# Optimization experiments

Hardware: AMD Instinct MI355X
Metric: run time of the kernel (lower is better)

The kernel has to match this reference:

```python
import jax, jax.numpy as jnp
import numpy as np

N, K, C, HID, G = 100000, 16, 64, 16, 128  # points, knn, channels, mlp hidden, voxel grid


def setup_inputs() -> dict:
    key = jax.random.key(0)
    ks = jax.random.split(key, 8)
    x_F = jax.random.normal(ks[0], (N, C), dtype=jnp.float32)
    idx = jax.random.randint(ks[1], (N, K), 0, N)  # knn neighbor indices

    # --- synthetic unique voxel coords + 3x3x3 sparse-conv neighbor map ---
    rng = np.random.default_rng(0)
    lin = rng.choice(G ** 3, size=N, replace=False)
    lut = np.full(G ** 3, -1, dtype=np.int64)
    lut[lin] = np.arange(N)
    xc, yc, zc = lin // (G * G), (lin // G) % G, lin % G
    nbrs = []
    for dx in (-1, 0, 1):
        for dy in (-1, 0, 1):
            for dz in (-1, 0, 1):
                nx, ny, nz = xc + dx, yc + dy, zc + dz
                valid = (nx >= 0) & (nx < G) & (ny >= 0) & (ny < G) & (nz >= 0) & (nz < G)
                nlin = np.clip(nx, 0, G - 1) * G * G + np.clip(ny, 0, G - 1) * G + np.clip(nz, 0, G - 1)
                nbrs.append(np.where(valid, lut[nlin], -1))
    conv_idx = jnp.asarray(np.stack(nbrs, axis=1))  # (N, 27), -1 = no neighbor voxel

    # --- learned params: shared channel MLP + sparse conv3d(2->1, k=3) weight ---
    W1 = jax.random.normal(ks[2], (C, HID), dtype=jnp.float32) / np.sqrt(C)
    b1 = jnp.zeros((HID,), dtype=jnp.float32)
    W2 = jax.random.normal(ks[3], (HID, C), dtype=jnp.float32) / np.sqrt(HID)
    b2 = jnp.zeros((C,), dtype=jnp.float32)
    conv_w = jax.random.normal(ks[4], (27, 2, 1), dtype=jnp.float32) / np.sqrt(27 * 2)
    return {"x_F": x_F, "W1": W1, "b1": b1, "W2": W2, "b2": b2,
            "conv_w": conv_w, "idx": idx, "conv_idx": conv_idx}


def reference(x_F, W1, b1, W2, b2, conv_w, idx, conv_idx):
    n = x_F.shape[0]

    def mlp(v):
        return jax.nn.relu(v @ W1 + b1) @ W2 + b2

    # channel attention: knn gather -> mean/max pool over k -> shared MLP gate
    g = x_F[idx]                                           # (n, k, c)
    gate = jax.nn.sigmoid(mlp(g.mean(axis=1)) + mlp(g.max(axis=1)))
    outse = x_F * gate                                     # (n, c)

    # spatial attention: pool over flattened (k*c), sparse conv3d(2->1)
    g2 = outse[idx].reshape(n, -1)                         # (n, k*c)
    z = jnp.stack([g2.mean(axis=1), g2.max(axis=1)], axis=1)  # (n, 2)
    mask = (conv_idx >= 0).astype(z.dtype)[..., None]      # (n, 27, 1)
    zn = z[jnp.clip(conv_idx, 0)] * mask                   # (n, 27, 2)
    convf = jnp.einsum('nkc,kco->no', zn, conv_w)          # (n, 1)
    return outse * jax.nn.sigmoid(convf)
```

## Files before the change

### kernel.cpp

```cpp
#include <hip/hip_runtime.h>
#include <math.h>

#define KNN 16
#define CH 64
#define HID 16
#define NEG_BIG (-3.402823466e+38f)

__device__ __forceinline__ float sigmoidf_(float x) {
    return 1.0f / (1.0f + __expf(-x));
}

__device__ __forceinline__ unsigned int pack_bf2(float a, float b) {
    unsigned int ua = __float_as_uint(a), ub = __float_as_uint(b);
    ua = (ua + 0x7FFFu + ((ua >> 16) & 1u)) >> 16;
    ub = (ub + 0x7FFFu + ((ub >> 16) & 1u)) & 0xFFFF0000u;
    return ua | ub;
}

__device__ __forceinline__ float4 bf4_to_f4(unsigned int lo, unsigned int hi) {
    float4 r;
    r.x = __uint_as_float(lo << 16);
    r.y = __uint_as_float(lo & 0xFFFF0000u);
    r.z = __uint_as_float(hi << 16);
    r.w = __uint_as_float(hi & 0xFFFF0000u);
    return r;
}

__device__ __forceinline__ void fold8_2(float A[8], float B[8], int sub) {
    #pragma unroll
    for (int m = 4; m >= 1; m >>= 1) {
        bool hi = (sub & m) != 0;
        #pragma unroll
        for (int i = 0; i < m; ++i) {
            float sA = hi ? A[i] : A[i + m], kA_ = hi ? A[i + m] : A[i];
            A[i] = kA_ + __shfl_xor(sA, m);
            float sB = hi ? B[i] : B[i + m], kB_ = hi ? B[i + m] : B[i];
            B[i] = kB_ + __shfl_xor(sB, m);
        }
    }
}

__global__ __launch_bounds__(256) void kX(const float4* __restrict__ xv,
                                          uint2* __restrict__ xb, int n16) {
    int i = blockIdx.x * 256 + threadIdx.x;
    if (i >= n16) return;
    float4 v = xv[i];
    uint2 r;
    r.x = pack_bf2(v.x, v.y);
    r.y = pack_bf2(v.z, v.w);
    xb[i] = r;
}

__global__ __launch_bounds__(256, 3) void kA(const float4* __restrict__ xv,
        const uint4* __restrict__ xb4,
        const float* __restrict__ W1, const float* __restrict__ b1,
        const float* __restrict__ W2, const float* __restrict__ b2,
        const int2* __restrict__ idx2,
        float4* __restrict__ outse, float2* __restrict__ rowstat, int n) {
    __shared__ float4 w1a[128];
    __shared__ float4 w1b[128];
    __shared__ float4 w2q[256];
    int t = threadIdx.x;
    if (t < 128) {
        int h = t >> 3, s = t & 7;
        float4 a, b;
        a.x = W1[(8 * s + 0) * HID + h];
        a.y = W1[(8 * s + 1) * HID + h];
        a.z = W1[(8 * s + 2) * HID + h];
        a.w = W1[(8 * s + 3) * HID + h];
        b.x = W1[(8 * s + 4) * HID + h];
        b.y = W1[(8 * s + 5) * HID + h];
        b.z = W1[(8 * s + 6) * HID + h];
        b.w = W1[(8 * s + 7) * HID + h];
        w1a[t] = a;
        w1b[t] = b;
    }
    w2q[t] = ((const float4*)W2)[t];
    __syncthreads();

    int p = blockIdx.x * 32 + (t >> 3);
    int sub = t & 7;
    if (p >= n) return;

    int2 jp = idx2[(size_t)p * 8 + sub];
    int jA[8], jB[8];
    #pragma unroll
    for (int s = 0; s < 8; ++s) {
        jA[s] = __shfl(jp.x, s, 8);
        jB[s] = __shfl(jp.y, s, 8);
    }

    uint4 va[8], vb[8];
    #pragma unroll
    for (int s = 0; s < 8; ++s) va[s] = xb4[(size_t)jA[s] * 8 + sub];
    #pragma unroll
    for (int s = 0; s < 8; ++s) vb[s] = xb4[(size_t)jB[s] * 8 + sub];
    float4 own0 = xv[(size_t)p * 16 + 2 * sub];
    float4 own1 = xv[(size_t)p * 16 + 2 * sub + 1];
    float b1a = b1[sub], b1b = b1[sub + 8];
    float4 bq0 = ((const float4*)b2)[2 * sub];
    float4 bq1 = ((const float4*)b2)[2 * sub + 1];
    __builtin_amdgcn_sched_barrier(0);

    float4 sumLo, sumHi, mxLo, mxHi;
    {
        float4 lo = bf4_to_f4(va[0].x, va[0].y);
        float4 hi = bf4_to_f4(va[0].z, va[0].w);
        sumLo = lo; mxLo = lo; sumHi = hi; mxHi = hi;
    }
    #pragma unroll
    for (int s = 1; s < 8; ++s) {
        float4 lo = bf4_to_f4(va[s].x, va[s].y);
        float4 hi = bf4_to_f4(va[s].z, va[s].w);
        sumLo.x += lo.x; sumLo.y += lo.y; sumLo.z += lo.z; sumLo.w += lo.w;
        sumHi.x += hi.x; sumHi.y += hi.y; sumHi.z += hi.z; sumHi.w += hi.w;
        mxLo.x = fmaxf(mxLo.x, lo.x); mxLo.y = fmaxf(mxLo.y, lo.y);
        mxLo.z = fmaxf(mxLo.z, lo.z); mxLo.w = fmaxf(mxLo.w, lo.w);
        mxHi.x = fmaxf(mxHi.x, hi.x); mxHi.y = fmaxf(mxHi.y, hi.y);
        mxHi.z = fmaxf(mxHi.z, hi.z); mxHi.w = fmaxf(mxHi.w, hi.w);
    }
    #pragma unroll
    for (int s = 0; s < 8; ++s) {
        float4 lo = bf4_to_f4(vb[s].x, vb[s].y);
        float4 hi = bf4_to_f4(vb[s].z, vb[s].w);
        sumLo.x += lo.x; sumLo.y += lo.y; sumLo.z += lo.z; sumLo.w += lo.w;
        sumHi.x += hi.x; sumHi.y += hi.y; sumHi.z += hi.z; sumHi.w += hi.w;
        mxLo.x = fmaxf(mxLo.x, lo.x); mxLo.y = fmaxf(mxLo.y, lo.y);
        mxLo.z = fmaxf(mxLo.z, lo.z); mxLo.w = fmaxf(mxLo.w, lo.w);
        mxHi.x = fmaxf(mxHi.x, hi.x); mxHi.y = fmaxf(mxHi.y, hi.y);
        mxHi.z = fmaxf(mxHi.z, hi.z); mxHi.w = fmaxf(mxHi.w, hi.w);
    }
    const float inv_k = 1.0f / KNN;
    float4 meLo = {sumLo.x * inv_k, sumLo.y * inv_k, sumLo.z * inv_k, sumLo.w * inv_k};
    float4 meHi = {sumHi.x * inv_k, sumHi.y * inv_k, sumHi.z * inv_k, sumHi.w * inv_k};

    float Hm_a, Hm_b, Hx_a, Hx_b;
    {
        float A[8], B[8];
        #pragma unroll
        for (int h = 0; h < 8; ++h) {
            float4 wa = w1a[h * 8 + sub], wb = w1b[h * 8 + sub];
            A[h] = meLo.x * wa.x + meLo.y * wa.y + meLo.z * wa.z + meLo.w * wa.w
                 + meHi.x * wb.x + meHi.y * wb.y + meHi.z * wb.z + meHi.w * wb.w;
            float4 wa2 = w1a[(h + 8) * 8 + sub], wb2 = w1b[(h + 8) * 8 + sub];
            B[h] = meLo.x * wa2.x + meLo.y * wa2.y + meLo.z * wa2.z + meLo.w * wa2.w
                 + meHi.x * wb2.x + meHi.y * wb2.y + meHi.z * wb2.z + meHi.w * wb2.w;
        }
        fold8_2(A, B, sub);
        Hm_a = A[0]; Hm_b = B[0];
    }
    {
        float A[8], B[8];
        #pragma unroll
        for (int h = 0; h < 8; ++h) {
            float4 wa = w1a[h * 8 + sub], wb = w1b[h * 8 + sub];
            A[h] = mxLo.x * wa.x + mxLo.y * wa.y + mxLo.z * wa.z + mxLo.w * wa.w
                 + mxHi.x * wb.x + mxHi.y * wb.y + mxHi.z * wb.z + mxHi.w * wb.w;
            float4 wa2 = w1a[(h + 8) * 8 + sub], wb2 = w1b[(h + 8) * 8 + sub];
            B[h] = mxLo.x * wa2.x + mxLo.y * wa2.y + mxLo.z * wa2.z + mxLo.w * wa2.w
                 + mxHi.x * wb2.x + mxHi.y * wb2.y + mxHi.z * wb2.z + mxHi.w * wb2.w;
        }
        fold8_2(A, B, sub);
        Hx_a = A[0]; Hx_b = B[0];
    }
    float H_a = fmaxf(Hm_a + b1a, 0.0f) + fmaxf(Hx_a + b1a, 0.0f);
    float H_b = fmaxf(Hm_b + b1b, 0.0f) + fmaxf(Hx_b + b1b, 0.0f);

    float4 a0 = {0.f, 0.f, 0.f, 0.f}, a1 = {0.f, 0.f, 0.f, 0.f};
    #pragma unroll
    for (int h = 0; h < 8; ++h) {
        float Hh = __shfl(H_a, h, 8);
        float4 w0 = w2q[h * 16 + 2 * sub], w1v = w2q[h * 16 + 2 * sub + 1];
        a0.x += Hh * w0.x; a0.y += Hh * w0.y; a0.z += Hh * w0.z; a0.w += Hh * w0.w;
        a1.x += Hh * w1v.x; a1.y += Hh * w1v.y; a1.z += Hh * w1v.z; a1.w += Hh * w1v.w;
    }
    #pragma unroll
    for (int h = 0; h < 8; ++h) {
        float Hh = __shfl(H_b, h, 8);
        float4 w0 = w2q[(h + 8) * 16 + 2 * sub], w1v = w2q[(h + 8) * 16 + 2 * sub + 1];
        a0.x += Hh * w0.x; a0.y += Hh * w0.y; a0.z += Hh * w0.z; a0.w += Hh * w0.w;
        a1.x += Hh * w1v.x; a1.y += Hh * w1v.y; a1.z += Hh * w1v.z; a1.w += Hh * w1v.w;
    }
    float4 o0, o1;
    o0.x = own0.x * sigmoidf_(a0.x + 2.0f * bq0.x);
    o0.y = own0.y * sigmoidf_(a0.y + 2.0f * bq0.y);
    o0.z = own0.z * sigmoidf_(a0.z + 2.0f * bq0.z);
    o0.w = own0.w * sigmoidf_(a0.w + 2.0f * bq0.w);
    o1.x = own1.x * sigmoidf_(a1.x + 2.0f * bq1.x);
    o1.y = own1.y * sigmoidf_(a1.y + 2.0f * bq1.y);
    o1.z = own1.z * sigmoidf_(a1.z + 2.0f * bq1.z);
    o1.w = own1.w * sigmoidf_(a1.w + 2.0f * bq1.w);
    outse[(size_t)p * 16 + 2 * sub] = o0;
    outse[(size_t)p * 16 + 2 * sub + 1] = o1;

    float sm = (o0.x + o0.y + o0.z + o0.w) + (o1.x + o1.y + o1.z + o1.w);
    float sx = fmaxf(fmaxf(fmaxf(o0.x, o0.y), fmaxf(o0.z, o0.w)),
                     fmaxf(fmaxf(o1.x, o1.y), fmaxf(o1.z, o1.w)));
    #pragma unroll
    for (int m = 4; m >= 1; m >>= 1) {
        sm += __shfl_xor(sm, m);
        sx = fmaxf(sx, __shfl_xor(sx, m));
    }
    if (sub == 0) rowstat[p] = make_float2(sm * (1.0f / 64.0f), sx);
}

__global__ __launch_bounds__(256) void kB(const int4* __restrict__ idxv,
        const float2* __restrict__ rowstat, float2* __restrict__ z, int n) {
    int t = blockIdx.x * 256 + threadIdx.x;
    int i = t >> 1, half = t & 1;
    if (i >= n) return;
    int4 a = idxv[(size_t)i * 4 + half * 2];
    int4 b = idxv[(size_t)i * 4 + half * 2 + 1];
    float2 s0 = rowstat[a.x], s1 = rowstat[a.y], s2 = rowstat[a.z], s3 = rowstat[a.w];
    float2 s4 = rowstat[b.x], s5 = rowstat[b.y], s6 = rowstat[b.z], s7 = rowstat[b.w];
    float zm = (s0.x + s1.x) + (s2.x + s3.x) + ((s4.x + s5.x) + (s6.x + s7.x));
    float zx = fmaxf(fmaxf(fmaxf(s0.y, s1.y), fmaxf(s2.y, s3.y)),
                     fmaxf(fmaxf(s4.y, s5.y), fmaxf(s6.y, s7.y)));
    zm += __shfl_xor(zm, 1);
    zx = fmaxf(zx, __shfl_xor(zx, 1));
    if (half == 0) z[i] = make_float2(zm * (1.0f / 16.0f), zx);
}

__global__ __launch_bounds__(256) void kC(const int* __restrict__ conv_idx,
        const float* __restrict__ conv_w, const float2* __restrict__ z,
        const float4* __restrict__ outse, float4* __restrict__ out, int n) {
    __shared__ float cw[54];
    __shared__ float sgate[256];
    if (threadIdx.x < 54) cw[threadIdx.x] = conv_w[threadIdx.x];
    __syncthreads();
    int base = blockIdx.x * 256;
    int i = base + threadIdx.x;
    if (i < n) {
        float acc = 0.0f;
        #pragma unroll
        for (int k = 0; k < 27; ++k) {
            int j = conv_idx[(size_t)i * 27 + k];
            int jc = j >= 0 ? j : 0;
            float msk = j >= 0 ? 1.0f : 0.0f;
            float2 zz = z[jc];
            acc += msk * (zz.x * cw[2 * k] + zz.y * cw[2 * k + 1]);
        }
        sgate[threadIdx.x] = sigmoidf_(acc);
    }
    __syncthreads();
    int npts = n - base; if (npts > 256) npts = 256;
    int tot = npts * 16;
    for (int q = threadIdx.x; q < tot; q += 256) {
        float s = sgate[q >> 4];
        float4 v = outse[(size_t)base * 16 + q];
        out[(size_t)base * 16 + q] = make_float4(v.x * s, v.y * s, v.z * s, v.w * s);
    }
}

extern "C" void kernel_launch(void* const* d_in, const int* in_sizes, int n_in,
                              void* d_out, int out_size, void* d_ws, size_t ws_size,
                              hipStream_t stream) {
    const float* x_F    = (const float*)d_in[0];
    const float* W1     = (const float*)d_in[1];
    const float* b1     = (const float*)d_in[2];
    const float* W2     = (const float*)d_in[3];
    const float* b2     = (const float*)d_in[4];
    const float* conv_w = (const float*)d_in[5];
    const int*   idx    = (const int*)d_in[6];
    const int*   cidx   = (const int*)d_in[7];
    int n = in_sizes[0] / CH;

    char* ws = (char*)d_ws;
    size_t off = 0;
    uint2*  xb      = (uint2*)(ws + off);  off += (size_t)n * CH * 2;
    float*  outse   = (float*)(ws + off);  off += (size_t)n * CH * 4;
    float2* rowstat = (float2*)(ws + off); off += (size_t)n * 8;
    float2* zz      = (float2*)(ws + off); off += (size_t)n * 8;

    int n16 = n * 16;
    kX<<<(n16 + 255) / 256, 256, 0, stream>>>((const float4*)x_F, xb, n16);
    int blkA = (n + 31) / 32;
    kA<<<blkA, 256, 0, stream>>>((const float4*)x_F, (const uint4*)xb,
                                 W1, b1, W2, b2, (const int2*)idx,
                                 (float4*)outse, rowstat, n);
    int blkB = (2 * n + 255) / 256;
    kB<<<blkB, 256, 0, stream>>>((const int4*)idx, rowstat, zz, n);
    int blkP = (n + 255) / 256;
    kC<<<blkP, 256, 0, stream>>>(cidx, conv_w, zz, (const float4*)outse,
                                 (float4*)d_out, n);
}
```

Before: 171.4 us.

## Fuse four kernels into one persistent cooperative kernel with grid syncs

Replaces the four separate launches (bf16 pack, channel attention, knn row-stat pooling, sparse conv gate) with a single cooperative persistent kernel. The kernel uses grid-stride loops and grid.sync() between phases. The aim is to remove per-launch overhead and inter-kernel gaps. In exchange it adds grid-wide barrier costs and raises the launch-bounds occupancy hint from 3 to 4, which may increase register pressure. The grid size is hardcoded as perCU*256 CUs, which assumes a 256-CU device.

```diff
diff --git a/kernel.cpp b/kernel.cpp
--- a/kernel.cpp
+++ b/kernel.cpp
@@ -1,5 +1,8 @@
 #include <hip/hip_runtime.h>
+#include <hip/hip_cooperative_groups.h>
 #include <math.h>
+
+namespace cg = cooperative_groups;
 
 #define KNN 16
 #define CH 64
@@ -40,27 +43,26 @@
     }
 }
 
-__global__ __launch_bounds__(256) void kX(const float4* __restrict__ xv,
-                                          uint2* __restrict__ xb, int n16) {
-    int i = blockIdx.x * 256 + threadIdx.x;
-    if (i >= n16) return;
-    float4 v = xv[i];
-    uint2 r;
-    r.x = pack_bf2(v.x, v.y);
-    r.y = pack_bf2(v.z, v.w);
-    xb[i] = r;
-}
-
-__global__ __launch_bounds__(256, 3) void kA(const float4* __restrict__ xv,
-        const uint4* __restrict__ xb4,
+__global__ __launch_bounds__(256, 4) void kFused(
+        const float4* __restrict__ xv, uint2* __restrict__ xb,
         const float* __restrict__ W1, const float* __restrict__ b1,
         const float* __restrict__ W2, const float* __restrict__ b2,
-        const int2* __restrict__ idx2,
-        float4* __restrict__ outse, float2* __restrict__ rowstat, int n) {
+        const int* __restrict__ idx, const int* __restrict__ cidx,
+        const float* __restrict__ conv_w,
+        float4* __restrict__ outse, float2* __restrict__ rowstat,
+        float2* __restrict__ zz, float4* __restrict__ out, int n) {
+    cg::grid_group grid = cg::this_grid();
+
     __shared__ float4 w1a[128];
     __shared__ float4 w1b[128];
     __shared__ float4 w2q[256];
+    __shared__ float cw[54];
+    __shared__ float sgate[256];
+
     int t = threadIdx.x;
+    const int gsz = gridDim.x * 256;
+    const int gid = blockIdx.x * 256 + t;
+
     if (t < 128) {
         int h = t >> 3, s = t & 7;
         float4 a, b;
@@ -75,180 +77,198 @@
         w1a[t] = a;
         w1b[t] = b;
     }
+    if (t < 54) cw[t] = conv_w[t];
     w2q[t] = ((const float4*)W2)[t];
     __syncthreads();
 
-    int p = blockIdx.x * 32 + (t >> 3);
-    int sub = t & 7;
-    if (p >= n) return;
-
-    int2 jp = idx2[(size_t)p * 8 + sub];
-    int jA[8], jB[8];
-    #pragma unroll
-    for (int s = 0; s < 8; ++s) {
-        jA[s] = __shfl(jp.x, s, 8);
-        jB[s] = __shfl(jp.y, s, 8);
-    }
-
-    uint4 va[8], vb[8];
-    #pragma unroll
-    for (int s = 0; s < 8; ++s) va[s] = xb4[(size_t)jA[s] * 8 + sub];
-    #pragma unroll
-    for (int s = 0; s < 8; ++s) vb[s] = xb4[(size_t)jB[s] * 8 + sub];
-    float4 own0 = xv[(size_t)p * 16 + 2 * sub];
-    float4 own1 = xv[(size_t)p * 16 + 2 * sub + 1];
-    float b1a = b1[sub], b1b = b1[sub + 8];
-    float4 bq0 = ((const float4*)b2)[2 * sub];
-    float4 bq1 = ((const float4*)b2)[2 * sub + 1];
-    __builtin_amdgcn_sched_barrier(0);
-
-    float4 sumLo, sumHi, mxLo, mxHi;
+    int n16 = n * 16;
+    for (int i = gid; i < n16; i += gsz) {
+        float4 v = xv[i];
+        uint2 r;
+        r.x = pack_bf2(v.x, v.y);
+        r.y = pack_bf2(v.z, v.w);
+        xb[i] = r;
+    }
+    grid.sync();
+
     {
-        float4 lo = bf4_to_f4(va[0].x, va[0].y);
-        float4 hi = bf4_to_f4(va[0].z, va[0].w);
-        sumLo = lo; mxLo = lo; sumHi = hi; mxHi = hi;
-    }
-    #pragma unroll
-    for (int s = 1; s < 8; ++s) {
-        float4 lo = bf4_to_f4(va[s].x, va[s].y);
-        float4 hi = bf4_to_f4(va[s].z, va[s].w);
-        sumLo.x += lo.x; sumLo.y += lo.y; sumLo.z += lo.z; sumLo.w += lo.w;
-        sumHi.x += hi.x; sumHi.y += hi.y; sumHi.z += hi.z; sumHi.w += hi.w;
-        mxLo.x = fmaxf(mxLo.x, lo.x); mxLo.y = fmaxf(mxLo.y, lo.y);
-        mxLo.z = fmaxf(mxLo.z, lo.z); mxLo.w = fmaxf(mxLo.w, lo.w);
-        mxHi.x = fmaxf(mxHi.x, hi.x); mxHi.y = fmaxf(mxHi.y, hi.y);
-        mxHi.z = fmaxf(mxHi.z, hi.z); mxHi.w = fmaxf(mxHi.w, hi.w);
-    }
-    #pragma unroll
-    for (int s = 0; s < 8; ++s) {
-        float4 lo = bf4_to_f4(vb[s].x, vb[s].y);
-        float4 hi = bf4_to_f4(vb[s].z, vb[s].w);
-        sumLo.x += lo.x; sumLo.y += lo.y; sumLo.z += lo.z; sumLo.w += lo.w;
-        sumHi.x += hi.x; sumHi.y += hi.y; sumHi.z += hi.z; sumHi.w += hi.w;
-        mxLo.x = fmaxf(mxLo.x, lo.x); mxLo.y = fmaxf(mxLo.y, lo.y);
-        mxLo.z = fmaxf(mxLo.z, lo.z); mxLo.w = fmaxf(mxLo.w, lo.w);
-        mxHi.x = fmaxf(mxHi.x, hi.x); mxHi.y = fmaxf(mxHi.y, hi.y);
-        mxHi.z = fmaxf(mxHi.z, hi.z); mxHi.w = fmaxf(mxHi.w, hi.w);
-    }
-    const float inv_k = 1.0f / KNN;
-    float4 meLo = {sumLo.x * inv_k, sumLo.y * inv_k, sumLo.z * inv_k, sumLo.w * inv_k};
-    float4 meHi = {sumHi.x * inv_k, sumHi.y * inv_k, sumHi.z * inv_k, sumHi.w * inv_k};
-
-    float Hm_a, Hm_b, Hx_a, Hx_b;
+        const uint4* xb4 = (const uint4*)xb;
+        const int2* idx2 = (const int2*)idx;
+        int sub = t & 7;
+        int nPG = (n + 31) / 32;
+        for (int pg = blockIdx.x; pg < nPG; pg += gridDim.x) {
+            int p = pg * 32 + (t >> 3);
+            if (p < n) {
+                int2 jp = idx2[(size_t)p * 8 + sub];
+                int jA[8], jB[8];
+                #pragma unroll
+                for (int s = 0; s < 8; ++s) {
+                    jA[s] = __shfl(jp.x, s, 8);
+                    jB[s] = __shfl(jp.y, s, 8);
+                }
+                uint4 va[8], vb[8];
+                #pragma unroll
+                for (int s = 0; s < 8; ++s) va[s] = xb4[(size_t)jA[s] * 8 + sub];
+                #pragma unroll
+                for (int s = 0; s < 8; ++s) vb[s] = xb4[(size_t)jB[s] * 8 + sub];
+                float4 own0 = xv[(size_t)p * 16 + 2 * sub];
+                float4 own1 = xv[(size_t)p * 16 + 2 * sub + 1];
+                float b1a = b1[sub], b1b = b1[sub + 8];
+                float4 bq0 = ((const float4*)b2)[2 * sub];
+                float4 bq1 = ((const float4*)b2)[2 * sub + 1];
+                __builtin_amdgcn_sched_barrier(0);
+
+                float4 sumLo, sumHi, mxLo, mxHi;
+                {
+                    float4 lo = bf4_to_f4(va[0].x, va[0].y);
+                    float4 hi = bf4_to_f4(va[0].z, va[0].w);
+                    sumLo = lo; mxLo = lo; sumHi = hi; mxHi = hi;
+                }
+                #pragma unroll
+                for (int s = 1; s < 8; ++s) {
+                    float4 lo = bf4_to_f4(va[s].x, va[s].y);
+                    float4 hi = bf4_to_f4(va[s].z, va[s].w);
+                    sumLo.x += lo.x; sumLo.y += lo.y; sumLo.z += lo.z; sumLo.w += lo.w;
+                    sumHi.x += hi.x; sumHi.y += hi.y; sumHi.z += hi.z; sumHi.w += hi.w;
+                    mxLo.x = fmaxf(mxLo.x, lo.x); mxLo.y = fmaxf(mxLo.y, lo.y);
+                    mxLo.z = fmaxf(mxLo.z, lo.z); mxLo.w = fmaxf(mxLo.w, lo.w);
+                    mxHi.x = fmaxf(mxHi.x, hi.x); mxHi.y = fmaxf(mxHi.y, hi.y);
+                    mxHi.z = fmaxf(mxHi.z, hi.z); mxHi.w = fmaxf(mxHi.w, hi.w);
+                }
+                #pragma unroll
+                for (int s = 0; s < 8; ++s) {
+                    float4 lo = bf4_to_f4(vb[s].x, vb[s].y);
+                    float4 hi = bf4_to_f4(vb[s].z, vb[s].w);
+                    sumLo.x += lo.x; sumLo.y += lo.y; sumLo.z += lo.z; sumLo.w += lo.w;
+                    sumHi.x += hi.x; sumHi.y += hi.y; sumHi.z += hi.z; sumHi.w += hi.w;
+                    mxLo.x = fmaxf(mxLo.x, lo.x); mxLo.y = fmaxf(mxLo.y, lo.y);
+                    mxLo.z = fmaxf(mxLo.z, lo.z); mxLo.w = fmaxf(mxLo.w, lo.w);
+                    mxHi.x = fmaxf(mxHi.x, hi.x); mxHi.y = fmaxf(mxHi.y, hi.y);
+                    mxHi.z = fmaxf(mxHi.z, hi.z); mxHi.w = fmaxf(mxHi.w, hi.w);
+                }
+                const float inv_k = 1.0f / KNN;
+                float4 meLo = {sumLo.x * inv_k, sumLo.y * inv_k, sumLo.z * inv_k, sumLo.w * inv_k};
+                float4 meHi = {sumHi.x * inv_k, sumHi.y * inv_k, sumHi.z * inv_k, sumHi.w * inv_k};
+
+                float Hm_a, Hm_b, Hx_a, Hx_b;
+                {
+                    float A[8], B[8];
+                    #pragma unroll
+                    for (int h = 0; h < 8; ++h) {
+                        float4 wa = w1a[h * 8 + sub], wb = w1b[h * 8 + sub];
+                        A[h] = meLo.x * wa.x + meLo.y * wa.y + meLo.z * wa.z + meLo.w * wa.w
+                             + meHi.x * wb.x + meHi.y * wb.y + meHi.z * wb.z + meHi.w * wb.w;
+                        float4 wa2 = w1a[(h + 8) * 8 + sub], wb2 = w1b[(h + 8) * 8 + sub];
+                        B[h] = meLo.x * wa2.x + meLo.y * wa2.y + meLo.z * wa2.z + meLo.w * wa2.w
+                             + meHi.x * wb2.x + meHi.y * wb2.y + meHi.z * wb2.z + meHi.w * wb2.w;
+                    }
+                    fold8_2(A, B, sub);
+                    Hm_a = A[0]; Hm_b = B[0];
+                }
+                {
+                    float A[8], B[8];
+                    #pragma unroll
+                    for (int h = 0; h < 8; ++h) {
+                        float4 wa = w1a[h * 8 + sub], wb = w1b[h * 8 + sub];
+                        A[h] = mxLo.x * wa.x + mxLo.y * wa.y + mxLo.z * wa.z + mxLo.w * wa.w
+                             + mxHi.x * wb.x + mxHi.y * wb.y + mxHi.z * wb.z + mxHi.w * wb.w;
+                        float4 wa2 = w1a[(h + 8) * 8 + sub], wb2 = w1b[(h + 8) * 8 + sub];
+                        B[h] = mxLo.x * wa2.x + mxLo.y * wa2.y + mxLo.z * wa2.z + mxLo.w * wa2.w
+                             + mxHi.x * wb2.x + mxHi.y * wb2.y + mxHi.z * wb2.z + mxHi.w * wb2.w;
+                    }
+                    fold8_2(A, B, sub);
+                    Hx_a = A[0]; Hx_b = B[0];
+                }
+                float H_a = fmaxf(Hm_a + b1a, 0.0f) + fmaxf(Hx_a + b1a, 0.0f);
+                float H_b = fmaxf(Hm_b + b1b, 0.0f) + fmaxf(Hx_b + b1b, 0.0f);
+
+                float4 a0 = {0.f, 0.f, 0.f, 0.f}, a1 = {0.f, 0.f, 0.f, 0.f};
+                #pragma unroll
+                for (int h = 0; h < 8; ++h) {
+                    float Hh = __shfl(H_a, h, 8);
+                    float4 w0 = w2q[h * 16 + 2 * sub], w1v = w2q[h * 16 + 2 * sub + 1];
+                    a0.x += Hh * w0.x; a0.y += Hh * w0.y; a0.z += Hh * w0.z; a0.w += Hh * w0.w;
+                    a1.x += Hh * w1v.x; a1.y += Hh * w1v.y; a1.z += Hh * w1v.z; a1.w += Hh * w1v.w;
+                }
+                #pragma unroll
+                for (int h = 0; h < 8; ++h) {
+                    float Hh = __shfl(H_b, h, 8);
+                    float4 w0 = w2q[(h + 8) * 16 + 2 * sub], w1v = w2q[(h + 8) * 16 + 2 * sub + 1];
+                    a0.x += Hh * w0.x; a0.y += Hh * w0.y; a0.z += Hh * w0.z; a0.w += Hh * w0.w;
+                    a1.x += Hh * w1v.x; a1.y += Hh * w1v.y; a1.z += Hh * w1v.z; a1.w += Hh * w1v.w;
+                }
+                float4 o0, o1;
+                o0.x = own0.x * sigmoidf_(a0.x + 2.0f * bq0.x);
+                o0.y = own0.y * sigmoidf_(a0.y + 2.0f * bq0.y);
+                o0.z = own0.z * sigmoidf_(a0.z + 2.0f * bq0.z);
+                o0.w = own0.w * sigmoidf_(a0.w + 2.0f * bq0.w);
+                o1.x = own1.x * sigmoidf_(a1.x + 2.0f * bq1.x);
+                o1.y = own1.y * sigmoidf_(a1.y + 2.0f * bq1.y);
+                o1.z = own1.z * sigmoidf_(a1.z + 2.0f * bq1.z);
+                o1.w = own1.w * sigmoidf_(a1.w + 2.0f * bq1.w);
+                outse[(size_t)p * 16 + 2 * sub] = o0;
+                outse[(size_t)p * 16 + 2 * sub + 1] = o1;
+
+                float sm = (o0.x + o0.y + o0.z + o0.w) + (o1.x + o1.y + o1.z + o1.w);
+                float sx = fmaxf(fmaxf(fmaxf(o0.x, o0.y), fmaxf(o0.z, o0.w)),
+                                 fmaxf(fmaxf(o1.x, o1.y), fmaxf(o1.z, o1.w)));
+                #pragma unroll
+                for (int m = 4; m >= 1; m >>= 1) {
+                    sm += __shfl_xor(sm, m);
+                    sx = fmaxf(sx, __shfl_xor(sx, m));
+                }
+                if (sub == 0) rowstat[p] = make_float2(sm * (1.0f / 64.0f), sx);
+            }
+        }
+    }
+    grid.sync();
+
     {
-        float A[8], B[8];
-        #pragma unroll
-        for (int h = 0; h < 8; ++h) {
-            float4 wa = w1a[h * 8 + sub], wb = w1b[h * 8 + sub];
-            A[h] = meLo.x * wa.x + meLo.y * wa.y + meLo.z * wa.z + meLo.w * wa.w
-                 + meHi.x * wb.x + meHi.y * wb.y + meHi.z * wb.z + meHi.w * wb.w;
-            float4 wa2 = w1a[(h + 8) * 8 + sub], wb2 = w1b[(h + 8) * 8 + sub];
-            B[h] = meLo.x * wa2.x + meLo.y * wa2.y + meLo.z * wa2.z + meLo.w * wa2.w
-                 + meHi.x * wb2.x + meHi.y * wb2.y + meHi.z * wb2.z + meHi.w * wb2.w;
+        const int4* idxv = (const int4*)idx;
+        int two_n = 2 * n;
+        for (int tt = gid; tt < two_n; tt += gsz) {
+            int i = tt >> 1, half = tt & 1;
+            int4 a = idxv[(size_t)i * 4 + half * 2];
+            int4 b = idxv[(size_t)i * 4 + half * 2 + 1];
+            float2 s0 = rowstat[a.x], s1 = rowstat[a.y], s2 = rowstat[a.z], s3 = rowstat[a.w];
+            float2 s4 = rowstat[b.x], s5 = rowstat[b.y], s6 = rowstat[b.z], s7 = rowstat[b.w];
+            float zm = (s0.x + s1.x) + (s2.x + s3.x) + ((s4.x + s5.x) + (s6.x + s7.x));
+            float zx = fmaxf(fmaxf(fmaxf(s0.y, s1.y), fmaxf(s2.y, s3.y)),
+                             fmaxf(fmaxf(s4.y, s5.y), fmaxf(s6.y, s7.y)));
+            zm += __shfl_xor(zm, 1);
+            zx = fmaxf(zx, __shfl_xor(zx, 1));
+            if (half == 0) zz[i] = make_float2(zm * (1.0f / 16.0f), zx);
         }
-        fold8_2(A, B, sub);
-        Hm_a = A[0]; Hm_b = B[0];
-    }
+    }
+    grid.sync();
+
     {
-        float A[8], B[8];
-        #pragma unroll
-        for (int h = 0; h < 8; ++h) {
-            float4 wa = w1a[h * 8 + sub], wb = w1b[h * 8 + sub];
-            A[h] = mxLo.x * wa.x + mxLo.y * wa.y + mxLo.z * wa.z + mxLo.w * wa.w
-                 + mxHi.x * wb.x + mxHi.y * wb.y + mxHi.z * wb.z + mxHi.w * wb.w;
-            float4 wa2 = w1a[(h + 8) * 8 + sub], wb2 = w1b[(h + 8) * 8 + sub];
-            B[h] = mxLo.x * wa2.x + mxLo.y * wa2.y + mxLo.z * wa2.z + mxLo.w * wa2.w
-                 + mxHi.x * wb2.x + mxHi.y * wb2.y + mxHi.z * wb2.z + mxHi.w * wb2.w;
+        int nCh = (n + 255) / 256;
+        for (int c = blockIdx.x; c < nCh; c += gridDim.x) {
+            int base = c * 256;
+            int i = base + t;
+            if (i < n) {
+                float acc = 0.0f;
+                #pragma unroll
+                for (int k = 0; k < 27; ++k) {
+                    int j = cidx[(size_t)i * 27 + k];
+                    int jc = j >= 0 ? j : 0;
+                    float msk = j >= 0 ? 1.0f : 0.0f;
+                    float2 zv = zz[jc];
+                    acc += msk * (zv.x * cw[2 * k] + zv.y * cw[2 * k + 1]);
+                }
+                sgate[t] = sigmoidf_(acc);
+            }
+            __syncthreads();
+            int npts = n - base; if (npts > 256) npts = 256;
+            int tot = npts * 16;
+            for (int q = t; q < tot; q += 256) {
+                float s = sgate[q >> 4];
+                float4 v = outse[(size_t)base * 16 + q];
+                out[(size_t)base * 16 + q] = make_float4(v.x * s, v.y * s, v.z * s, v.w * s);
+            }
+            __syncthreads();
         }
-        fold8_2(A, B, sub);
-        Hx_a = A[0]; Hx_b = B[0];
-    }
-    float H_a = fmaxf(Hm_a + b1a, 0.0f) + fmaxf(Hx_a + b1a, 0.0f);
-    float H_b = fmaxf(Hm_b + b1b, 0.0f) + fmaxf(Hx_b + b1b, 0.0f);
-
-    float4 a0 = {0.f, 0.f, 0.f, 0.f}, a1 = {0.f, 0.f, 0.f, 0.f};
-    #pragma unroll
-    for (int h = 0; h < 8; ++h) {
-        float Hh = __shfl(H_a, h, 8);
-        float4 w0 = w2q[h * 16 + 2 * sub], w1v = w2q[h * 16 + 2 * sub + 1];
-        a0.x += Hh * w0.x; a0.y += Hh * w0.y; a0.z += Hh * w0.z; a0.w += Hh * w0.w;
-        a1.x += Hh * w1v.x; a1.y += Hh * w1v.y; a1.z += Hh * w1v.z; a1.w += Hh * w1v.w;
-    }
-    #pragma unroll
-    for (int h = 0; h < 8; ++h) {
-        float Hh = __shfl(H_b, h, 8);
-        float4 w0 = w2q[(h + 8) * 16 + 2 * sub], w1v = w2q[(h + 8) * 16 + 2 * sub + 1];
-        a0.x += Hh * w0.x; a0.y += Hh * w0.y; a0.z += Hh * w0.z; a0.w += Hh * w0.w;
-        a1.x += Hh * w1v.x; a1.y += Hh * w1v.y; a1.z += Hh * w1v.z; a1.w += Hh * w1v.w;
-    }
-    float4 o0, o1;
-    o0.x = own0.x * sigmoidf_(a0.x + 2.0f * bq0.x);
-    o0.y = own0.y * sigmoidf_(a0.y + 2.0f * bq0.y);
-    o0.z = own0.z * sigmoidf_(a0.z + 2.0f * bq0.z);
-    o0.w = own0.w * sigmoidf_(a0.w + 2.0f * bq0.w);
-    o1.x = own1.x * sigmoidf_(a1.x + 2.0f * bq1.x);
-    o1.y = own1.y * sigmoidf_(a1.y + 2.0f * bq1.y);
-    o1.z = own1.z * sigmoidf_(a1.z + 2.0f * bq1.z);
-    o1.w = own1.w * sigmoidf_(a1.w + 2.0f * bq1.w);
-    outse[(size_t)p * 16 + 2 * sub] = o0;
-    outse[(size_t)p * 16 + 2 * sub + 1] = o1;
-
-    float sm = (o0.x + o0.y + o0.z + o0.w) + (o1.x + o1.y + o1.z + o1.w);
-    float sx = fmaxf(fmaxf(fmaxf(o0.x, o0.y), fmaxf(o0.z, o0.w)),
-                     fmaxf(fmaxf(o1.x, o1.y), fmaxf(o1.z, o1.w)));
-    #pragma unroll
-    for (int m = 4; m >= 1; m >>= 1) {
-        sm += __shfl_xor(sm, m);
-        sx = fmaxf(sx, __shfl_xor(sx, m));
-    }
-    if (sub == 0) rowstat[p] = make_float2(sm * (1.0f / 64.0f), sx);
-}
-
-__global__ __launch_bounds__(256) void kB(const int4* __restrict__ idxv,
-        const float2* __restrict__ rowstat, float2* __restrict__ z, int n) {
-    int t = blockIdx.x * 256 + threadIdx.x;
-    int i = t >> 1, half = t & 1;
-    if (i >= n) return;
-    int4 a = idxv[(size_t)i * 4 + half * 2];
-    int4 b = idxv[(size_t)i * 4 + half * 2 + 1];
-    float2 s0 = rowstat[a.x], s1 = rowstat[a.y], s2 = rowstat[a.z], s3 = rowstat[a.w];
-    float2 s4 = rowstat[b.x], s5 = rowstat[b.y], s6 = rowstat[b.z], s7 = rowstat[b.w];
-    float zm = (s0.x + s1.x) + (s2.x + s3.x) + ((s4.x + s5.x) + (s6.x + s7.x));
-    float zx = fmaxf(fmaxf(fmaxf(s0.y, s1.y), fmaxf(s2.y, s3.y)),
-                     fmaxf(fmaxf(s4.y, s5.y), fmaxf(s6.y, s7.y)));
-    zm += __shfl_xor(zm, 1);
-    zx = fmaxf(zx, __shfl_xor(zx, 1));
-    if (half == 0) z[i] = make_float2(zm * (1.0f / 16.0f), zx);
-}
-
-__global__ __launch_bounds__(256) void kC(const int* __restrict__ conv_idx,
-        const float* __restrict__ conv_w, const float2* __restrict__ z,
-        const float4* __restrict__ outse, float4* __restrict__ out, int n) {
-    __shared__ float cw[54];
-    __shared__ float sgate[256];
-    if (threadIdx.x < 54) cw[threadIdx.x] = conv_w[threadIdx.x];
-    __syncthreads();
-    int base = blockIdx.x * 256;
-    int i = base + threadIdx.x;
-    if (i < n) {
-        float acc = 0.0f;
-        #pragma unroll
-        for (int k = 0; k < 27; ++k) {
-            int j = conv_idx[(size_t)i * 27 + k];
-            int jc = j >= 0 ? j : 0;
-            float msk = j >= 0 ? 1.0f : 0.0f;
-            float2 zz = z[jc];
-            acc += msk * (zz.x * cw[2 * k] + zz.y * cw[2 * k + 1]);
-        }
-        sgate[threadIdx.x] = sigmoidf_(acc);
-    }
-    __syncthreads();
-    int npts = n - base; if (npts > 256) npts = 256;
-    int tot = npts * 16;
-    for (int q = threadIdx.x; q < tot; q += 256) {
-        float s = sgate[q >> 4];
-        float4 v = outse[(size_t)base * 16 + q];
-        out[(size_t)base * 16 + q] = make_float4(v.x * s, v.y * s, v.z * s, v.w * s);
     }
 }
 
@@ -272,15 +292,21 @@
     float2* rowstat = (float2*)(ws + off); off += (size_t)n * 8;
     float2* zz      = (float2*)(ws + off); off += (size_t)n * 8;
 
-    int n16 = n * 16;
-    kX<<<(n16 + 255) / 256, 256, 0, stream>>>((const float4*)x_F, xb, n16);
-    int blkA = (n + 31) / 32;
-    kA<<<blkA, 256, 0, stream>>>((const float4*)x_F, (const uint4*)xb,
-                                 W1, b1, W2, b2, (const int2*)idx,
-                                 (float4*)outse, rowstat, n);
-    int blkB = (2 * n + 255) / 256;
-    kB<<<blkB, 256, 0, stream>>>((const int4*)idx, rowstat, zz, n);
-    int blkP = (n + 255) / 256;
-    kC<<<blkP, 256, 0, stream>>>(cidx, conv_w, zz, (const float4*)outse,
-                                 (float4*)d_out, n);
-}
+    const float4* xv = (const float4*)x_F;
+    float4* outsev = (float4*)outse;
+    float4* outv = (float4*)d_out;
+
+    int perCU = 0;
+    hipError_t e = hipOccupancyMaxActiveBlocksPerMultiprocessor(
+        &perCU, reinterpret_cast<const void*>(kFused), 256, 0);
+    if (e != hipSuccess || perCU < 1) perCU = 2;
+    if (perCU > 8) perCU = 8;
+    int grid = perCU * 256;
+
+    void* args[] = {(void*)&xv, (void*)&xb, (void*)&W1, (void*)&b1, (void*)&W2,
+                    (void*)&b2, (void*)&idx, (void*)&cidx, (void*)&conv_w,
+                    (void*)&outsev, (void*)&rowstat, (void*)&zz, (void*)&outv,
+                    (void*)&n};
+    hipLaunchCooperativeKernel(reinterpret_cast<void*>(kFused),
+                               dim3(grid), dim3(256), args, 0, stream);
+}
```

After: 486.7 us. +183.9%, slower.
